# Kernel optimization log

Hardware: AMD Instinct MI355X
Metric: run time of the kernel (lower is better)

The kernel has to match this reference:

```python
import jax, jax.numpy as jnp
import numpy as np

B, S, D, H, DFF = 2, 2048, 1024, 16, 4096
DK = D // H
EPS = 1e-6
MASK_FILL = -1.0  # original code uses -1**9 == -1 (precedence bug), NOT -1e9


def layernorm(x, gamma, beta):
    # original: (x - mean) / (std + eps), std unbiased (torch default ddof=1), scalar gamma/beta
    mean = jnp.mean(x, axis=-1, keepdims=True)
    std = jnp.std(x, axis=-1, keepdims=True, ddof=1)
    return gamma * (x - mean) / (std + EPS) + beta


def setup_inputs() -> dict:
    key = jax.random.key(0)
    ks = jax.random.split(key, 12)
    sc = 0.02
    return {
        "x": jax.random.normal(ks[0], (B, S, D), jnp.float32),
        "src_mask": jnp.ones((B, 1, 1, S), jnp.int32),
        "wq": jax.random.normal(ks[1], (D, D), jnp.float32) * sc,
        "bq": jnp.zeros((D,), jnp.float32),
        "wk": jax.random.normal(ks[2], (D, D), jnp.float32) * sc,
        "bk": jnp.zeros((D,), jnp.float32),
        "wv": jax.random.normal(ks[3], (D, D), jnp.float32) * sc,
        "bv": jnp.zeros((D,), jnp.float32),
        "wo": jax.random.normal(ks[4], (D, D), jnp.float32) * sc,
        "bo": jnp.zeros((D,), jnp.float32),
        "w1": jax.random.normal(ks[5], (D, DFF), jnp.float32) * sc,
        "b1": jnp.zeros((DFF,), jnp.float32),
        "w2": jax.random.normal(ks[6], (DFF, D), jnp.float32) * sc,
        "b2": jnp.zeros((D,), jnp.float32),
        "g1": jnp.ones((), jnp.float32),
        "be1": jnp.zeros((), jnp.float32),
        "g2": jnp.ones((), jnp.float32),
        "be2": jnp.zeros((), jnp.float32),
    }


def reference(x, src_mask, wq, bq, wk, bk, wv, bv, wo, bo,
              w1, b1, w2, b2, g1, be1, g2, be2):
    # --- residual 1: pre-LN self-attention ---
    xn = layernorm(x, g1, be1)
    q = (xn @ wq + bq).reshape(B, S, H, DK).transpose(0, 2, 1, 3)  # [B,H,S,DK]
    k = (xn @ wk + bk).reshape(B, S, H, DK).transpose(0, 2, 1, 3)
    v = (xn @ wv + bv).reshape(B, S, H, DK).transpose(0, 2, 1, 3)
    scores = jnp.einsum('bhqd,bhkd->bhqk', q, k) / jnp.sqrt(jnp.float32(DK))
    scores = jnp.where(src_mask == 0, MASK_FILL, scores)
    attn = jax.nn.softmax(scores, axis=-1)
    ctx = jnp.einsum('bhqk,bhkd->bhqd', attn, v)
    ctx = ctx.transpose(0, 2, 1, 3).reshape(B, S, D)
    attn_out = ctx @ wo + bo
    x = x + attn_out  # dropout is identity in eval

    # --- residual 2: pre-LN feed-forward ---
    xn = layernorm(x, g2, be2)
    h = jax.nn.relu(xn @ w1 + b1)
    ff_out = h @ w2 + b2
    return x + ff_out
```

## Files before the change

### kernel.cpp

```cpp
#include <hip/hip_runtime.h>

typedef unsigned short u16;
typedef __bf16 bf16x8 __attribute__((ext_vector_type(8)));
typedef float f32x4 __attribute__((ext_vector_type(4)));
typedef float f32x16 __attribute__((ext_vector_type(16)));

#define AS1U(p) ((__attribute__((address_space(1))) unsigned int*)(p))
#define AS3U(p) ((__attribute__((address_space(3))) unsigned int*)(p))

__device__ __forceinline__ u16 f2bf(float f) {
  union { float f; unsigned int i; } c; c.f = f;
  return (u16)((c.i + 0x7FFFu + ((c.i >> 16) & 1u)) >> 16);
}
__device__ __forceinline__ u16 f2bf_trunc(float f) {
  union { float f; unsigned int i; } c; c.f = f;
  return (u16)(c.i >> 16);
}
__device__ __forceinline__ unsigned cvt_pk_bf16(float lo, float hi) {
  unsigned r;
  asm("v_cvt_pk_bf16_f32 %0, %1, %2" : "=v"(r) : "v"(lo), "v"(hi));
  return r;
}
__device__ __forceinline__ void plswap(unsigned& a, unsigned& b) {
  asm("v_permlane32_swap_b32 %0, %1" : "+v"(a), "+v"(b));
}

template <int OMODE>
__global__ __launch_bounds__(512, 2) void gemm8(
    const u16* __restrict__ A, long lda,
    const u16* __restrict__ B, long ldb,
    void* __restrict__ Cv, long ldc,
    int K, const float* __restrict__ bias,
    const float* __restrict__ res, long ldres, int relu) {
  __shared__ u16 As[2][256 * 64];
  __shared__ u16 Bs[2][256 * 64];
  const int t = threadIdx.x;
  const int w = t >> 6, l = t & 63;
  const int hi = l >> 5, lq = l & 31;
  const int wm = w >> 2, wn = w & 3;
  const long row0 = (long)blockIdx.x * 256;
  const long col0 = (long)blockIdx.y * 256;

  auto stageU = [&](int bb, int unit, int k0) {
    const u16* src = (unit < 2) ? B : A;
    const long ld = (unit < 2) ? ldb : lda;
    const long base0 = (unit < 2) ? col0 : row0;
    u16* dst = (unit < 2) ? &Bs[bb][0] : &As[bb][0];
    const int h = unit & 1;
#pragma unroll
    for (int i = 0; i < 2; i++) {
      int s = t + i * 512;
      int r = h * 128 + (s >> 3), c = s & 7;
      __builtin_amdgcn_global_load_lds(AS1U(src + (base0 + r) * ld + k0 + ((c ^ (r & 7)) * 8)),
                                       AS3U(dst + ((long)(r * 8 + c)) * 8), 16, 0, 0);
    }
  };

  f32x16 acc[4][2] = {};
  const int NT = K >> 6;

  stageU(0, 0, 0); stageU(0, 1, 0); stageU(0, 2, 0); stageU(0, 3, 0);
  if (NT > 1) stageU(1, 0, 64);
  asm volatile("s_waitcnt vmcnt(2)" ::: "memory");
  __builtin_amdgcn_sched_barrier(0);
  __builtin_amdgcn_s_barrier();
  __builtin_amdgcn_sched_barrier(0);

  bf16x8 bfr[2][4];
  for (int tt = 0; tt < NT; tt++) {
    const int cb = tt & 1, nb = cb ^ 1;
    const int kN = (tt + 1) << 6, kN2 = (tt + 2) << 6;
#pragma unroll
    for (int mi = 0; mi < 4; mi++) {
      bf16x8 afr[4];
      {
        const int r = wm * 128 + mi * 32 + lq;
#pragma unroll
        for (int kk = 0; kk < 4; kk++)
          afr[kk] = *(const bf16x8*)&As[cb][(r * 8 + ((kk * 2 + hi) ^ (r & 7))) * 8];
      }
      if (mi == 0) {
#pragma unroll
        for (int nj = 0; nj < 2; nj++) {
          const int r = wn * 64 + nj * 32 + lq;
#pragma unroll
          for (int kk = 0; kk < 4; kk++)
            bfr[nj][kk] = *(const bf16x8*)&Bs[cb][(r * 8 + ((kk * 2 + hi) ^ (r & 7))) * 8];
        }
      }
      if (mi == 0) { if (tt + 1 < NT) stageU(nb, 1, kN); }
      else if (mi == 1) { if (tt + 1 < NT) stageU(nb, 2, kN); }
      else if (mi == 2) { if (tt + 1 < NT) stageU(nb, 3, kN); }
      else {
        if (tt + 2 < NT) stageU(cb, 0, kN2);
        if (tt < NT - 2) asm volatile("s_waitcnt vmcnt(2)" ::: "memory");
        else             asm volatile("s_waitcnt vmcnt(0)" ::: "memory");
      }
      __builtin_amdgcn_sched_barrier(0);
      __builtin_amdgcn_s_barrier();
      __builtin_amdgcn_sched_barrier(0);
      __builtin_amdgcn_s_setprio(1);
#pragma unroll
      for (int kk = 0; kk < 4; kk++)
#pragma unroll
        for (int nj = 0; nj < 2; nj++)
          acc[mi][nj] = __builtin_amdgcn_mfma_f32_32x32x16_bf16(afr[kk], bfr[nj][kk], acc[mi][nj], 0, 0, 0);
      __builtin_amdgcn_s_setprio(0);
      __builtin_amdgcn_sched_barrier(0);
      __builtin_amdgcn_s_barrier();
      __builtin_amdgcn_sched_barrier(0);
    }
  }

#pragma unroll
  for (int nj = 0; nj < 2; nj++) {
    const long gn = col0 + wn * 64 + nj * 32 + lq;
    const float bv = bias ? bias[gn] : 0.0f;
#pragma unroll
    for (int mi = 0; mi < 4; mi++) {
#pragma unroll
      for (int g = 0; g < 16; g++) {
        const long gm = row0 + wm * 128 + mi * 32 + (g & 3) + 8 * (g >> 2) + 4 * hi;
        float v = acc[mi][nj][g] + bv;
        if (relu && v < 0.0f) v = 0.0f;
        if (res) v += res[gm * ldres + gn];
        if (OMODE == 0) ((float*)Cv)[gm * ldc + gn] = v;
        else ((u16*)Cv)[gm * ldc + gn] = f2bf(v);
      }
    }
  }
}

template <int BM, int BN, int BK, int OMODE>
__global__ __launch_bounds__(256) void gemm_bt(
    const u16* __restrict__ A, long lda,
    const u16* __restrict__ B, long ldb,
    void* __restrict__ Cv, long ldc,
    int K, float scale, const float* __restrict__ bias,
    const float* __restrict__ res, long ldres, int relu) {
  constexpr int WN = (BN == 128) ? 64 : 32;
  constexpr int MI = 4, NJ = WN / 16;
  constexpr int KK = BK / 32;
  __shared__ u16 As0[BM * BK], As1[BM * BK];
  __shared__ u16 Bs0[BN * BK], Bs1[BN * BK];
  const int t = threadIdx.x;
  const int w = t >> 6, l = t & 63;
  const int wr = w >> 1, wc = w & 1;
  const int quad = l >> 4, mlo = l & 15;
  const long row0 = (long)blockIdx.x * BM;
  const long col0 = (long)blockIdx.y * BN;

  f32x4 acc[MI][NJ] = {};

  auto stage = [&](u16 (&Ad)[BM * BK], u16 (&Bd)[BN * BK], int k0) {
    if (BK == 32) {
#pragma unroll
      for (int i = 0; i < BM / 64; i++) {
        int s = t + i * 256, r = s >> 2, c = s & 3;
        const u16* g = A + (row0 + r) * lda + k0 + c * 8;
        __builtin_amdgcn_global_load_lds(AS1U(g), AS3U(&Ad[s * 8]), 16, 0, 0);
      }
#pragma unroll
      for (int i = 0; i < BN / 64; i++) {
        int s = t + i * 256, r = s >> 2, c = s & 3;
        const u16* g = B + (col0 + r) * ldb + k0 + c * 8;
        __builtin_amdgcn_global_load_lds(AS1U(g), AS3U(&Bd[s * 8]), 16, 0, 0);
      }
    } else {
#pragma unroll
      for (int i = 0; i < BM / 32; i++) {
        int s = t + i * 256, r = s >> 3, c = s & 7;
        const u16* g = A + (row0 + r) * lda + k0 + (c ^ (r & 7)) * 8;
        __builtin_amdgcn_global_load_lds(AS1U(g), AS3U(&Ad[s * 8]), 16, 0, 0);
      }
#pragma unroll
      for (int i = 0; i < BN / 32; i++) {
        int s = t + i * 256, r = s >> 3, c = s & 7;
        const u16* g = B + (col0 + r) * ldb + k0 + (c ^ (r & 7)) * 8;
        __builtin_amdgcn_global_load_lds(AS1U(g), AS3U(&Bd[s * 8]), 16, 0, 0);
      }
    }
  };
  auto compute = [&](const u16 (&Asr)[BM * BK], const u16 (&Bsr)[BN * BK]) {
#pragma unroll
    for (int kk = 0; kk < KK; kk++) {
      bf16x8 a[MI], b[NJ];
#pragma unroll
      for (int i = 0; i < MI; i++) {
        int r = wr * 64 + i * 16 + mlo;
        a[i] = (BK == 32) ? *(const bf16x8*)&Asr[(r * 4 + quad) * 8]
                          : *(const bf16x8*)&Asr[(r * 8 + ((kk * 4 + quad) ^ (r & 7))) * 8];
      }
#pragma unroll
      for (int j = 0; j < NJ; j++) {
        int r = wc * WN + j * 16 + mlo;
        b[j] = (BK == 32) ? *(const bf16x8*)&Bsr[(r * 4 + quad) * 8]
                          : *(const bf16x8*)&Bsr[(r * 8 + ((kk * 4 + quad) ^ (r & 7))) * 8];
      }
#pragma unroll
      for (int i = 0; i < MI; i++)
#pragma unroll
        for (int j = 0; j < NJ; j++)
          acc[i][j] = __builtin_amdgcn_mfma_f32_16x16x32_bf16(a[i], b[j], acc[i][j], 0, 0, 0);
    }
  };

  stage(As0, Bs0, 0);
  for (int k0 = 0; k0 < K; k0 += 2 * BK) {
    __syncthreads();
    stage(As1, Bs1, k0 + BK);
    compute(As0, Bs0);
    __syncthreads();
    if (k0 + 2 * BK < K) stage(As0, Bs0, k0 + 2 * BK);
    compute(As1, Bs1);
  }

#pragma unroll
  for (int i = 0; i < MI; i++) {
#pragma unroll
    for (int j = 0; j < NJ; j++) {
      const long gn = col0 + wc * WN + j * 16 + mlo;
      const float bv = bias ? bias[gn] : 0.0f;
#pragma unroll
      for (int r = 0; r < 4; r++) {
        const long gm = row0 + wr * 64 + i * 16 + quad * 4 + r;
        float v = acc[i][j][r] * scale + bv;
        if (relu && v < 0.0f) v = 0.0f;
        if (res) v += res[gm * ldres + gn];
        if (OMODE == 0) ((float*)Cv)[gm * ldc + gn] = v;
        else ((u16*)Cv)[gm * ldc + gn] = f2bf(v);
      }
    }
  }
}

__global__ __launch_bounds__(256, 2) void flash_attn(
    const u16* __restrict__ QKV, const u16* __restrict__ VT,
    const int* __restrict__ mask, u16* __restrict__ ctx) {
  __shared__ u16 Ks[2][64 * 64];
  __shared__ u16 Vs[2][64 * 64];
  const int t = threadIdx.x;
  const int w = t >> 6, l = t & 63;
  const int hi = l >> 5, lq = l & 31, rx = lq & 7;
  const int z = blockIdx.z, b = z >> 4, h = z & 15;
  const long q0 = (long)blockIdx.x * 128;
  const u16* Qg = QKV + (long)b * (2048L * 3072) + h * 64;
  const u16* Kg = Qg + 1024;
  const u16* Vg = VT + (long)b * (1024L * 2048) + (long)(h * 64) * 2048;
  const int* mrow = mask + b * 2048;

#pragma unroll
  for (int i = 0; i < 2; i++) {
    int s = t + i * 256, r = s >> 3, c = s & 7;
    __builtin_amdgcn_global_load_lds(AS1U(Kg + (long)r * 3072 + (c ^ (r & 7)) * 8),
                                     AS3U(&Ks[0][s * 8]), 16, 0, 0);
    __builtin_amdgcn_global_load_lds(AS1U(Vg + (long)r * 2048 + (c ^ (r & 7)) * 8),
                                     AS3U(&Vs[0][s * 8]), 16, 0, 0);
  }

  const float CS = 0.125f * 1.44269504f;
  const float CM = -1.44269504f;

  bf16x8 aq[4];
#pragma unroll
  for (int kk = 0; kk < 4; kk++) {
    const u16* g = Qg + (q0 + w * 32 + lq) * 3072 + kk * 16 + hi * 8;
    union { uint4 u; bf16x8 v; u16 s[8]; } cc; cc.u = *(const uint4*)g;
#pragma unroll
    for (int e = 0; e < 8; e++) {
      union { unsigned u; float f; } qf; qf.u = (unsigned)cc.s[e] << 16;
      cc.s[e] = f2bf(qf.f * CS);
    }
    aq[kk] = cc.v;
  }

  unsigned am = 0;
  for (int it = 0; it < 32; ++it) {
    unsigned long long bmv = __ballot(mrow[it * 64 + l] != 0);
    am |= ((bmv == ~0ull) ? 1u : 0u) << it;
  }

  f32x16 o[2] = {}, den = {};
  union { u16 s[8]; bf16x8 v; } ones;
#pragma unroll
  for (int e = 0; e < 8; e++) ones.s[e] = 0x3F80;

  for (int it = 0; it < 32; ++it) {
    const int cur = it & 1;
    __syncthreads();
    if (it + 1 < 32) {
      const int nb = 1 - cur;
      const u16* Kg2 = Kg + (long)(it + 1) * 64 * 3072;
      const u16* Vg2 = Vg + (it + 1) * 64;
#pragma unroll
      for (int i2 = 0; i2 < 2; i2++) {
        int s = t + i2 * 256, r = s >> 3, c = s & 7;
        __builtin_amdgcn_global_load_lds(AS1U(Kg2 + (long)r * 3072 + (c ^ (r & 7)) * 8),
                                         AS3U(&Ks[nb][s * 8]), 16, 0, 0);
        __builtin_amdgcn_global_load_lds(AS1U(Vg2 + (long)r * 2048 + (c ^ (r & 7)) * 8),
                                         AS3U(&Vs[nb][s * 8]), 16, 0, 0);
      }
    }
    const bool allone = (am >> it) & 1u;
    unsigned long long bm = ~0ull;
    if (!allone) bm = __ballot(mrow[it * 64 + l] != 0);

    f32x16 sa[2];
    __builtin_amdgcn_s_setprio(1);
#pragma unroll
    for (int kt = 0; kt < 2; kt++) {
      f32x16 s0 = {};
      const int rk = kt * 32 + lq;
#pragma unroll
      for (int kk = 0; kk < 4; kk++) {
        bf16x8 ak = *(const bf16x8*)&Ks[cur][(rk * 8 + ((2 * kk + hi) ^ rx)) * 8];
        s0 = __builtin_amdgcn_mfma_f32_32x32x16_bf16(ak, aq[kk], s0, 0, 0, 0);
      }
      sa[kt] = s0;
    }
    __builtin_amdgcn_s_setprio(0);

#pragma unroll
    for (int kt = 0; kt < 2; kt++) {
      float p[16];
      if (allone) {
#pragma unroll
        for (int g = 0; g < 16; g++) p[g] = __builtin_amdgcn_exp2f(sa[kt][g]);
      } else {
#pragma unroll
        for (int g = 0; g < 16; g++) {
          const int k = kt * 32 + (g & 3) + 8 * (g >> 2) + 4 * hi;
          const float s = ((bm >> k) & 1) ? sa[kt][g] : CM;
          p[g] = __builtin_amdgcn_exp2f(s);
        }
      }
      unsigned wd[4][2];
#pragma unroll
      for (int g = 0; g < 4; g++) {
        wd[g][0] = cvt_pk_bf16(p[4 * g + 0], p[4 * g + 1]);
        wd[g][1] = cvt_pk_bf16(p[4 * g + 2], p[4 * g + 3]);
      }
#pragma unroll
      for (int c = 0; c < 2; c++) {
        plswap(wd[2 * c][0], wd[2 * c + 1][0]);
        plswap(wd[2 * c][1], wd[2 * c + 1][1]);
        union { unsigned u[4]; bf16x8 v; } pa;
        pa.u[0] = wd[2 * c][0];
        pa.u[1] = wd[2 * c][1];
        pa.u[2] = wd[2 * c + 1][0];
        pa.u[3] = wd[2 * c + 1][1];
        const int cg = kt * 2 + c;
        __builtin_amdgcn_s_setprio(1);
#pragma unroll
        for (int dt = 0; dt < 2; dt++) {
          const int rv = dt * 32 + lq;
          bf16x8 bv = *(const bf16x8*)&Vs[cur][(rv * 8 + ((2 * cg + hi) ^ rx)) * 8];
          o[dt] = __builtin_amdgcn_mfma_f32_32x32x16_bf16(pa.v, bv, o[dt], 0, 0, 0);
        }
        den = __builtin_amdgcn_mfma_f32_32x32x16_bf16(pa.v, ones.v, den, 0, 0, 0);
        __builtin_amdgcn_s_setprio(0);
      }
    }
  }

  u16* cb = ctx + (long)b * (2048L * 1024) + (q0 + w * 32) * 1024 + h * 64;
#pragma unroll
  for (int g = 0; g < 16; g++) {
    const int row = (g & 3) + 8 * (g >> 2) + 4 * hi;
    const float inv = 1.0f / den[g];
    cb[(long)row * 1024 + lq] = f2bf(o[0][g] * inv);
    cb[(long)row * 1024 + 32 + lq] = f2bf(o[1][g] * inv);
  }
}

__device__ __forceinline__ void ln_row(const float* __restrict__ x, u16* __restrict__ y,
                                       const float* __restrict__ g, const float* __restrict__ b,
                                       long row, float* ss, float* s2) {
  const float* xr = x + row * 1024;
  float v[4];
  float s = 0.f, sq = 0.f;
#pragma unroll
  for (int i = 0; i < 4; i++) {
    float f = xr[threadIdx.x + i * 256];
    v[i] = f; s += f; sq += f * f;
  }
#pragma unroll
  for (int o = 32; o > 0; o >>= 1) { s += __shfl_xor(s, o, 64); sq += __shfl_xor(sq, o, 64); }
  const int w = threadIdx.x >> 6;
  if ((threadIdx.x & 63) == 0) { ss[w] = s; s2[w] = sq; }
  __syncthreads();
  s = ss[0] + ss[1] + ss[2] + ss[3];
  sq = s2[0] + s2[1] + s2[2] + s2[3];
  const float mean = s * (1.0f / 1024.0f);
  float var = (sq - s * mean) * (1.0f / 1023.0f);
  var = fmaxf(var, 0.0f);
  const float sc = g[0] / (sqrtf(var) + 1e-6f);
  const float be = b[0];
#pragma unroll
  for (int i = 0; i < 4; i++)
    y[row * 1024 + threadIdx.x + i * 256] = f2bf((v[i] - mean) * sc + be);
}

__global__ __launch_bounds__(256) void ln_kernel(const float* __restrict__ x, u16* __restrict__ y,
                                                 const float* __restrict__ g, const float* __restrict__ b) {
  __shared__ float ss[4], s2[4];
  ln_row(x, y, g, b, blockIdx.x, ss, s2);
}

__global__ __launch_bounds__(256) void prep_kernel(
    const float* __restrict__ x, const float* __restrict__ g1, const float* __restrict__ be1,
    const float* __restrict__ wq, const float* __restrict__ wk, const float* __restrict__ wv,
    const float* __restrict__ wo, const float* __restrict__ w1, const float* __restrict__ w2,
    const float* __restrict__ bq, const float* __restrict__ bk, const float* __restrict__ bv,
    u16* __restrict__ xnH, u16* __restrict__ WqkvT, u16* __restrict__ woT,
    u16* __restrict__ w1T, u16* __restrict__ w2T, float* __restrict__ biasQKV) {
  __shared__ float tile[32][33];
  __shared__ float ss[4], s2[4];
  const int bid = blockIdx.x;
  if (bid >= 12300) {
    ln_row(x, xnH, g1, be1, bid - 12300, ss, s2);
    return;
  }
  if (bid >= 12288) {
    const int i = (bid - 12288) * 256 + threadIdx.x;
    if (i < 3072) biasQKV[i] = (i < 1024) ? bq[i] : ((i < 2048) ? bk[i - 1024] : bv[i - 2048]);
    return;
  }
  const float* in; u16* out; long ldin, ldo; int ti, tiles_x;
  if (bid < 1024)      { in = wq; out = WqkvT;                     ldin = 1024; ldo = 1024; ti = bid;        tiles_x = 32; }
  else if (bid < 2048) { in = wk; out = WqkvT + (size_t)1024*1024; ldin = 1024; ldo = 1024; ti = bid - 1024; tiles_x = 32; }
  else if (bid < 3072) { in = wv; out = WqkvT + (size_t)2048*1024; ldin = 1024; ldo = 1024; ti = bid - 2048; tiles_x = 32; }
  else if (bid < 4096) { in = wo; out = woT;                       ldin = 1024; ldo = 1024; ti = bid - 3072; tiles_x = 32; }
  else if (bid < 8192) { in = w1; out = w1T;                       ldin = 4096; ldo = 1024; ti = bid - 4096; tiles_x = 128; }
  else                 { in = w2; out = w2T;                       ldin = 1024; ldo = 4096; ti = bid - 8192; tiles_x = 32; }
  const int bx = (ti % tiles_x) * 32, by = (ti / tiles_x) * 32;
  const int tx = threadIdx.x & 31, ty = threadIdx.x >> 5;
#pragma unroll
  for (int i = 0; i < 32; i += 8) tile[ty + i][tx] = in[(long)(by + ty + i) * ldin + bx + tx];
  __syncthreads();
#pragma unroll
  for (int i = 0; i < 32; i += 8)
    out[(long)(bx + ty + i) * ldo + by + tx] = f2bf(tile[tx][ty + i]);
}

__global__ __launch_bounds__(256) void ttrans1(const u16* __restrict__ in, long ldin, long siz,
                                               u16* __restrict__ out, long ldo, long soz) {
  __shared__ u16 tile[32][33];
  const long zi = (long)blockIdx.z * siz, zo = (long)blockIdx.z * soz;
  const int bx = blockIdx.x * 32, by = blockIdx.y * 32;
  const int tx = threadIdx.x & 31, ty = threadIdx.x >> 5;
#pragma unroll
  for (int i = 0; i < 32; i += 8)
    tile[ty + i][tx] = in[zi + (long)(by + ty + i) * ldin + bx + tx];
  __syncthreads();
#pragma unroll
  for (int i = 0; i < 32; i += 8)
    out[zo + (long)(bx + ty + i) * ldo + by + tx] = tile[tx][ty + i];
}

extern "C" void kernel_launch(void* const* d_in, const int* in_sizes, int n_in,
                              void* d_out, int out_size, void* d_ws, size_t ws_size,
                              hipStream_t stream) {
  const float* x   = (const float*)d_in[0];
  const int*   msk = (const int*)d_in[1];
  const float* wq  = (const float*)d_in[2];
  const float* bq  = (const float*)d_in[3];
  const float* wk  = (const float*)d_in[4];
  const float* bk  = (const float*)d_in[5];
  const float* wv  = (const float*)d_in[6];
  const float* bv  = (const float*)d_in[7];
  const float* wo  = (const float*)d_in[8];
  const float* bo  = (const float*)d_in[9];
  const float* w1  = (const float*)d_in[10];
  const float* b1  = (const float*)d_in[11];
  const float* w2  = (const float*)d_in[12];
  const float* b2  = (const float*)d_in[13];
  const float* g1  = (const float*)d_in[14];
  const float* be1 = (const float*)d_in[15];
  const float* g2  = (const float*)d_in[16];
  const float* be2 = (const float*)d_in[17];
  float* out = (float*)d_out;

  char* basep = (char*)d_ws;
  size_t off = 0;
  auto au = [&](size_t nelem) -> u16* {
    u16* r = (u16*)(basep + off);
    off += ((nelem * 2) + 255) & ~(size_t)255;
    return r;
  };
  auto afp = [&](size_t nelem) -> float* {
    float* r = (float*)(basep + off);
    off += ((nelem * 4) + 255) & ~(size_t)255;
    return r;
  };

  u16* xnH  = au((size_t)4096 * 1024);
  u16* QKV  = au((size_t)4096 * 3072);
  u16* VTH  = au((size_t)2 * 1024 * 2048);
  u16* ctxH = au((size_t)4096 * 1024);
  float* x1 = afp((size_t)4096 * 1024);
  u16* hb   = au((size_t)4096 * 4096);
  u16* WqkvT = au((size_t)3072 * 1024);
  u16* woT  = au((size_t)1024 * 1024);
  u16* w1T  = au((size_t)4096 * 1024);
  u16* w2T  = au((size_t)1024 * 4096);
  float* biasQKV = afp(3072);

  const dim3 blk(256);
  const dim3 blk5(512);

  prep_kernel<<<16396, blk, 0, stream>>>(x, g1, be1, wq, wk, wv, wo, w1, w2,
                                         bq, bk, bv, xnH, WqkvT, woT, w1T, w2T, biasQKV);

  gemm8<2><<<dim3(16, 12), blk5, 0, stream>>>(
      xnH, 1024, WqkvT, 1024, QKV, 3072, 1024,
      biasQKV, (const float*)0, 0, 0);

  ttrans1<<<dim3(32, 64, 2), blk, 0, stream>>>(
      QKV + 2048, 3072, (long)2048 * 3072, VTH, 2048, (long)1024 * 2048);

  flash_attn<<<dim3(16, 1, 32), blk, 0, stream>>>(QKV, VTH, msk, ctxH);

  gemm_bt<128, 64, 64, 0><<<dim3(32, 16), blk, 0, stream>>>(
      ctxH, 1024, woT, 1024, x1, 1024, 1024, 1.0f, bo, x, 1024, 0);

  ln_kernel<<<4096, blk, 0, stream>>>(x1, xnH, g2, be2);

  gemm8<2><<<dim3(16, 16), blk5, 0, stream>>>(
      xnH, 1024, w1T, 1024, hb, 4096, 1024,
      b1, (const float*)0, 0, 1);

  gemm_bt<128, 64, 64, 0><<<dim3(32, 16), blk, 0, stream>>>(
      hb, 4096, w2T, 4096, out, 1024, 4096, 1.0f, b2, x1, 1024, 0);
}
```

Before: 343.1 us.

## Fuse V transpose into QKV GEMM epilogue, drop separate transpose kernel

```diff
diff --git a/kernel.cpp b/kernel.cpp
--- a/kernel.cpp
+++ b/kernel.cpp
@@ -11,10 +11,6 @@
 __device__ __forceinline__ u16 f2bf(float f) {
   union { float f; unsigned int i; } c; c.f = f;
   return (u16)((c.i + 0x7FFFu + ((c.i >> 16) & 1u)) >> 16);
-}
-__device__ __forceinline__ u16 f2bf_trunc(float f) {
-  union { float f; unsigned int i; } c; c.f = f;
-  return (u16)(c.i >> 16);
 }
 __device__ __forceinline__ unsigned cvt_pk_bf16(float lo, float hi) {
   unsigned r;
@@ -31,7 +27,8 @@
     const u16* __restrict__ B, long ldb,
     void* __restrict__ Cv, long ldc,
     int K, const float* __restrict__ bias,
-    const float* __restrict__ res, long ldres, int relu) {
+    const float* __restrict__ res, long ldres, int relu,
+    u16* __restrict__ vtp) {
   __shared__ u16 As[2][256 * 64];
   __shared__ u16 Bs[2][256 * 64];
   const int t = threadIdx.x;
@@ -110,6 +107,49 @@
       __builtin_amdgcn_s_barrier();
       __builtin_amdgcn_sched_barrier(0);
     }
+  }
+
+  if (OMODE == 2 && vtp != nullptr && col0 >= 2048) {
+    u16* vt = vtp;
+    const int bb = (int)(row0 >> 11);
+    const int tok0 = (int)(row0 & 2047);
+    const long vcol0 = col0 - 2048;
+    u16* shp = &As[0][0];
+#pragma unroll
+    for (int ph = 0; ph < 4; ph++) {
+      const int rh = ph >> 1, ch = ph & 1;
+      if (wm == rh && (wn >> 1) == ch) {
+        const int cbs = (wn & 1) * 64;
+#pragma unroll
+        for (int nj = 0; nj < 2; nj++) {
+          const long gn = col0 + wn * 64 + nj * 32 + lq;
+          const float bv = bias ? bias[gn] : 0.0f;
+#pragma unroll
+          for (int mi = 0; mi < 4; mi++) {
+#pragma unroll
+            for (int g = 0; g < 16; g++) {
+              const int rr = mi * 32 + (g & 3) + 8 * (g >> 2) + 4 * hi;
+              shp[rr * 130 + cbs + nj * 32 + lq] = f2bf(acc[mi][nj][g] + bv);
+            }
+          }
+        }
+      }
+      __syncthreads();
+      {
+        const int rbase = w * 16;
+#pragma unroll
+        for (int rr = 0; rr < 16; rr++) {
+          const int r = rbase + rr;
+          const u16 a0 = shp[(l * 2 + 0) * 130 + r];
+          const u16 a1 = shp[(l * 2 + 1) * 130 + r];
+          const unsigned pk = (unsigned)a0 | ((unsigned)a1 << 16);
+          const long vrow = vcol0 + ch * 128 + r;
+          *(unsigned*)(vt + (long)bb * (1024L * 2048) + vrow * 2048 + tok0 + rh * 128 + l * 2) = pk;
+        }
+      }
+      __syncthreads();
+    }
+    return;
   }
 
 #pragma unroll
@@ -153,32 +193,17 @@
   f32x4 acc[MI][NJ] = {};
 
   auto stage = [&](u16 (&Ad)[BM * BK], u16 (&Bd)[BN * BK], int k0) {
-    if (BK == 32) {
-#pragma unroll
-      for (int i = 0; i < BM / 64; i++) {
-        int s = t + i * 256, r = s >> 2, c = s & 3;
-        const u16* g = A + (row0 + r) * lda + k0 + c * 8;
-        __builtin_amdgcn_global_load_lds(AS1U(g), AS3U(&Ad[s * 8]), 16, 0, 0);
-      }
-#pragma unroll
-      for (int i = 0; i < BN / 64; i++) {
-        int s = t + i * 256, r = s >> 2, c = s & 3;
-        const u16* g = B + (col0 + r) * ldb + k0 + c * 8;
-        __builtin_amdgcn_global_load_lds(AS1U(g), AS3U(&Bd[s * 8]), 16, 0, 0);
-      }
-    } else {
-#pragma unroll
-      for (int i = 0; i < BM / 32; i++) {
-        int s = t + i * 256, r = s >> 3, c = s & 7;
-        const u16* g = A + (row0 + r) * lda + k0 + (c ^ (r & 7)) * 8;
-        __builtin_amdgcn_global_load_lds(AS1U(g), AS3U(&Ad[s * 8]), 16, 0, 0);
-      }
-#pragma unroll
-      for (int i = 0; i < BN / 32; i++) {
-        int s = t + i * 256, r = s >> 3, c = s & 7;
-        const u16* g = B + (col0 + r) * ldb + k0 + (c ^ (r & 7)) * 8;
-        __builtin_amdgcn_global_load_lds(AS1U(g), AS3U(&Bd[s * 8]), 16, 0, 0);
-      }
+#pragma unroll
+    for (int i = 0; i < BM / 32; i++) {
+      int s = t + i * 256, r = s >> 3, c = s & 7;
+      const u16* g = A + (row0 + r) * lda + k0 + (c ^ (r & 7)) * 8;
+      __builtin_amdgcn_global_load_lds(AS1U(g), AS3U(&Ad[s * 8]), 16, 0, 0);
+    }
+#pragma unroll
+    for (int i = 0; i < BN / 32; i++) {
+      int s = t + i * 256, r = s >> 3, c = s & 7;
+      const u16* g = B + (col0 + r) * ldb + k0 + (c ^ (r & 7)) * 8;
+      __builtin_amdgcn_global_load_lds(AS1U(g), AS3U(&Bd[s * 8]), 16, 0, 0);
     }
   };
   auto compute = [&](const u16 (&Asr)[BM * BK], const u16 (&Bsr)[BN * BK]) {
@@ -188,14 +213,12 @@
 #pragma unroll
       for (int i = 0; i < MI; i++) {
         int r = wr * 64 + i * 16 + mlo;
-        a[i] = (BK == 32) ? *(const bf16x8*)&Asr[(r * 4 + quad) * 8]
-                          : *(const bf16x8*)&Asr[(r * 8 + ((kk * 4 + quad) ^ (r & 7))) * 8];
+        a[i] = *(const bf16x8*)&Asr[(r * 8 + ((kk * 4 + quad) ^ (r & 7))) * 8];
       }
 #pragma unroll
       for (int j = 0; j < NJ; j++) {
         int r = wc * WN + j * 16 + mlo;
-        b[j] = (BK == 32) ? *(const bf16x8*)&Bsr[(r * 4 + quad) * 8]
-                          : *(const bf16x8*)&Bsr[(r * 8 + ((kk * 4 + quad) ^ (r & 7))) * 8];
+        b[j] = *(const bf16x8*)&Bsr[(r * 8 + ((kk * 4 + quad) ^ (r & 7))) * 8];
       }
 #pragma unroll
       for (int i = 0; i < MI; i++)
@@ -441,21 +464,6 @@
 #pragma unroll
   for (int i = 0; i < 32; i += 8)
     out[(long)(bx + ty + i) * ldo + by + tx] = f2bf(tile[tx][ty + i]);
-}
-
-__global__ __launch_bounds__(256) void ttrans1(const u16* __restrict__ in, long ldin, long siz,
-                                               u16* __restrict__ out, long ldo, long soz) {
-  __shared__ u16 tile[32][33];
-  const long zi = (long)blockIdx.z * siz, zo = (long)blockIdx.z * soz;
-  const int bx = blockIdx.x * 32, by = blockIdx.y * 32;
-  const int tx = threadIdx.x & 31, ty = threadIdx.x >> 5;
-#pragma unroll
-  for (int i = 0; i < 32; i += 8)
-    tile[ty + i][tx] = in[zi + (long)(by + ty + i) * ldin + bx + tx];
-  __syncthreads();
-#pragma unroll
-  for (int i = 0; i < 32; i += 8)
-    out[zo + (long)(bx + ty + i) * ldo + by + tx] = tile[tx][ty + i];
 }
 
 extern "C" void kernel_launch(void* const* d_in, const int* in_sizes, int n_in,
@@ -514,10 +522,7 @@
 
   gemm8<2><<<dim3(16, 12), blk5, 0, stream>>>(
       xnH, 1024, WqkvT, 1024, QKV, 3072, 1024,
-      biasQKV, (const float*)0, 0, 0);
-
-  ttrans1<<<dim3(32, 64, 2), blk, 0, stream>>>(
-      QKV + 2048, 3072, (long)2048 * 3072, VTH, 2048, (long)1024 * 2048);
+      biasQKV, (const float*)0, 0, 0, VTH);
 
   flash_attn<<<dim3(16, 1, 32), blk, 0, stream>>>(QKV, VTH, msk, ctxH);
 
@@ -528,7 +533,7 @@
 
   gemm8<2><<<dim3(16, 16), blk5, 0, stream>>>(
       xnH, 1024, w1T, 1024, hb, 4096, 1024,
-      b1, (const float*)0, 0, 1);
+      b1, (const float*)0, 0, 1, (u16*)0);
 
   gemm_bt<128, 64, 64, 0><<<dim3(32, 16), blk, 0, stream>>>(
       hb, 4096, w2T, 4096, out, 1024, 4096, 1.0f, b2, x1, 1024, 0);
```

Measured after the change: 346.7 us. Within noise of the previous version (+1.0%).
